# Optimization experiments

Measured on AMD Instinct MI355X. Metric: run time of the kernel, lower is better.

The kernel has to match this reference:

```python
import jax, jax.numpy as jnp
import numpy as np

EPS = 1e-6
NUM_HEADS = 12


def _layernorm(x, eps=EPS):
    m = jnp.mean(x, axis=-1, keepdims=True)
    v = jnp.var(x, axis=-1, keepdims=True)
    return (x - m) * jax.lax.rsqrt(v + eps)


def _rmsnorm(x, w, eps=EPS):
    ms = jnp.mean(jnp.square(x), axis=-1, keepdims=True)
    return x * jax.lax.rsqrt(ms + eps) * w


def _rope_interleaved(x, cos, sin):
    # x: [B, L, H, hd]; cos/sin: [L, hd//2]; is_neox_style=False (interleaved pairs)
    x1 = x[..., 0::2]
    x2 = x[..., 1::2]
    c = cos[None, :, None, :]
    s = sin[None, :, None, :]
    o1 = x1 * c - x2 * s
    o2 = x1 * s + x2 * c
    return jnp.stack([o1, o2], axis=-1).reshape(x.shape)


def _attention(q, k, v, mask=None):
    # q: [B, Lq, H, hd], k/v: [B, Lk, H, hd]
    hd = q.shape[-1]
    scale = 1.0 / jnp.sqrt(jnp.asarray(hd, q.dtype))
    scores = jnp.einsum('blhd,bmhd->bhlm', q, k) * scale
    if mask is not None:
        scores = jnp.where(mask[None, None], scores, jnp.finfo(scores.dtype).min)
    p = jax.nn.softmax(scores, axis=-1)
    return jnp.einsum('bhlm,bmhd->blhd', p, v)


def setup_inputs() -> dict:
    key = jax.random.key(0)
    B, F, FS, D, FF, LC = 1, 2, 1560, 1536, 8960, 512
    L = F * FS
    hd = D // NUM_HEADS
    ks = jax.random.split(key, 32)
    i = iter(range(32))
    n = lambda shape, s=0.02: jax.random.normal(ks[next(i)], shape, jnp.float32) * s
    inp = {
        'hidden_states': n((B, L, D), 1.0),
        'encoder_hidden_states': n((B, LC, D), 1.0),
        'temb': n((B, F, 6, D), 1.0),
    }
    pos = jnp.arange(L, dtype=jnp.float32)
    inv = 1.0 / (10000.0 ** (jnp.arange(hd // 2, dtype=jnp.float32) / (hd // 2)))
    ang = pos[:, None] * inv[None, :]
    inp['cos'] = jnp.cos(ang)
    inp['sin'] = jnp.sin(ang)
    fidx = jnp.arange(L) // FS
    inp['attn_mask'] = fidx[:, None] >= fidx[None, :]  # frame-level block-causal
    # params
    inp['sst'] = n((1, 6, D), 1.0 / np.sqrt(D))
    for name in ['wq', 'wk', 'wv', 'wo']:
        inp[name] = n((D, D))
    for name in ['bq', 'bk', 'bv', 'bo']:
        inp[name] = jnp.zeros((D,), jnp.float32)
    inp['nq_w'] = jnp.ones((D,), jnp.float32)
    inp['nk_w'] = jnp.ones((D,), jnp.float32)
    inp['ln2_g'] = jnp.ones((D,), jnp.float32)
    inp['ln2_b'] = jnp.zeros((D,), jnp.float32)
    for name in ['cwq', 'cwk', 'cwv', 'cwo']:
        inp[name] = n((D, D))
    for name in ['cbq', 'cbk', 'cbv', 'cbo']:
        inp[name] = jnp.zeros((D,), jnp.float32)
    inp['cnq_w'] = jnp.ones((D,), jnp.float32)
    inp['cnk_w'] = jnp.ones((D,), jnp.float32)
    inp['w1'] = n((D, FF))
    inp['b1'] = jnp.zeros((FF,), jnp.float32)
    inp['w2'] = n((FF, D))
    inp['b2'] = jnp.zeros((D,), jnp.float32)
    return inp


def reference(hidden_states, encoder_hidden_states, temb, cos, sin, attn_mask,
              sst, wq, bq, wk, bk, wv, bv, wo, bo, nq_w, nk_w, ln2_g, ln2_b,
              cwq, cbq, cwk, cbk, cwv, cbv, cwo, cbo, cnq_w, cnk_w,
              w1, b1, w2, b2):
    B, L, D = hidden_states.shape
    F = temb.shape[1]
    FS = L // F
    H = NUM_HEADS
    hd = D // H

    e = sst[:, None] + temb  # [B, F, 6, D]
    shift_msa, scale_msa, gate_msa = e[:, :, 0], e[:, :, 1], e[:, :, 2]
    c_shift, c_scale, c_gate = e[:, :, 3], e[:, :, 4], e[:, :, 5]

    # --- self attention ---
    nh = _layernorm(hidden_states).reshape(B, F, FS, D)
    nh = (nh * (1.0 + scale_msa[:, :, None]) + shift_msa[:, :, None]).reshape(B, L, D)
    q = _rmsnorm(nh @ wq + bq, nq_w).reshape(B, L, H, hd)
    k = _rmsnorm(nh @ wk + bk, nk_w).reshape(B, L, H, hd)
    v = (nh @ wv + bv).reshape(B, L, H, hd)
    q = _rope_interleaved(q, cos, sin)
    k = _rope_interleaved(k, cos, sin)
    attn_out = _attention(q, k, v, attn_mask).reshape(B, L, D) @ wo + bo

    h = hidden_states + (attn_out.reshape(B, F, FS, D) * gate_msa[:, :, None]).reshape(B, L, D)
    norm_h = _layernorm(h) * ln2_g + ln2_b  # null shift/scale

    # --- cross attention ---
    LC = encoder_hidden_states.shape[1]
    cq = _rmsnorm(norm_h @ cwq + cbq, cnq_w).reshape(B, L, H, hd)
    ck = _rmsnorm(encoder_hidden_states @ cwk + cbk, cnk_w).reshape(B, LC, H, hd)
    cv = (encoder_hidden_states @ cwv + cbv).reshape(B, LC, H, hd)
    cross_out = _attention(cq, ck, cv).reshape(B, L, D) @ cwo + cbo

    h = h + cross_out  # gate = 1
    norm_h = _layernorm(h).reshape(B, F, FS, D)
    norm_h = (norm_h * (1.0 + c_scale[:, :, None]) + c_shift[:, :, None]).reshape(B, L, D)

    # --- ffn ---
    ff = jax.nn.gelu(norm_h @ w1 + b1, approximate=True) @ w2 + b2
    h = h + (ff.reshape(B, F, FS, D) * c_gate[:, :, None]).reshape(B, L, D)
    return h
```

## Files before the change

### kernel.cpp

```cpp
#include <hip/hip_runtime.h>
#include <hip/hip_bf16.h>
#include <math.h>

typedef __bf16 bf16;
typedef __bf16 bf16x8 __attribute__((ext_vector_type(8)));
typedef float  f32x4  __attribute__((ext_vector_type(4)));
typedef unsigned int u32;

#define DMODEL 1536
#define NHEADS 12
#define HD 128
#define HDH 64

__device__ __forceinline__ void async16(const void* g, void* l) {
  __builtin_amdgcn_global_load_lds((const __attribute__((address_space(1))) u32*)g,
                                   (__attribute__((address_space(3))) u32*)l, 16, 0, 0);
}

__device__ inline void block_reduce2(float& a, float& b) {
  __shared__ float sa[4], sb[4];
  #pragma unroll
  for (int off = 32; off; off >>= 1) {
    a += __shfl_xor(a, off);
    b += __shfl_xor(b, off);
  }
  int w = threadIdx.x >> 6;
  if ((threadIdx.x & 63) == 0) { sa[w] = a; sb[w] = b; }
  __syncthreads();
  a = sa[0] + sa[1] + sa[2] + sa[3];
  b = sb[0] + sb[1] + sb[2] + sb[3];
  __syncthreads();
}

__global__ __launch_bounds__(256)
void ln_kernel(const float* __restrict__ X, bf16* __restrict__ Y,
               const float* __restrict__ sst, const float* __restrict__ temb,
               const float* __restrict__ g, const float* __restrict__ bvec,
               int jshift, int jscale, int FS, int mode)
{
  int row = blockIdx.x;
  const float* x = X + (size_t)row * DMODEL;
  float v[6];
  float s1 = 0.f, s2 = 0.f;
  #pragma unroll
  for (int i = 0; i < 6; i++) {
    float t = x[threadIdx.x + i * 256];
    v[i] = t; s1 += t; s2 += t * t;
  }
  block_reduce2(s1, s2);
  float mean = s1 * (1.f / DMODEL);
  float var  = s2 * (1.f / DMODEL) - mean * mean;
  float rs = rsqrtf(var + 1e-6f);
  int f = row / FS;
  bf16* y = Y + (size_t)row * DMODEL;
  #pragma unroll
  for (int i = 0; i < 6; i++) {
    int d = threadIdx.x + i * 256;
    float t = (v[i] - mean) * rs;
    float o;
    if (mode == 0) {
      float sc = sst[jscale * DMODEL + d] + temb[(f * 6 + jscale) * DMODEL + d];
      float sh = sst[jshift * DMODEL + d] + temb[(f * 6 + jshift) * DMODEL + d];
      o = t * (1.f + sc) + sh;
    } else {
      o = t * g[d] + bvec[d];
    }
    y[d] = (bf16)o;
  }
}

__global__ __launch_bounds__(256)
void rms_rope_kernel(const float* __restrict__ P, int S, long long MN,
                     const bf16* __restrict__ Xb, int RS, int CO,
                     const float* __restrict__ bias, bf16* __restrict__ Y,
                     const float* __restrict__ w,
                     const float* __restrict__ cosb, const float* __restrict__ sinb,
                     int dorope, float oscale)
{
  __shared__ float rowbuf[DMODEL];
  int row = blockIdx.x;
  float v[6];
  float s2 = 0.f, dummy = 0.f;
  if (Xb) {
    const bf16* x = Xb + (size_t)row * RS + CO;
    #pragma unroll
    for (int i = 0; i < 6; i++) {
      int d = threadIdx.x + i * 256;
      float t = (float)x[d];
      v[i] = t; rowbuf[d] = t; s2 += t * t;
    }
  } else {
    const float* x = P + (size_t)row * RS + CO;
    #pragma unroll
    for (int i = 0; i < 6; i++) {
      int d = threadIdx.x + i * 256;
      float t = bias[d];
      for (int s = 0; s < S; s++) t += x[(size_t)s * MN + d];
      v[i] = t; rowbuf[d] = t; s2 += t * t;
    }
  }
  __syncthreads();
  block_reduce2(s2, dummy);
  float rs = rsqrtf(s2 * (1.f / DMODEL) + 1e-6f) * oscale;
  bf16* y = Y + (size_t)row * DMODEL;
  if (dorope) {
    #pragma unroll
    for (int i = 0; i < 3; i++) {
      int p = threadIdx.x + i * 256;
      int d0 = 2 * p, d1 = 2 * p + 1;
      float y0 = rowbuf[d0] * rs * w[d0];
      float y1 = rowbuf[d1] * rs * w[d1];
      int ih = p & 63;
      float c = cosb[(size_t)row * HDH + ih];
      float s = sinb[(size_t)row * HDH + ih];
      y[d0] = (bf16)(y0 * c - y1 * s);
      y[d1] = (bf16)(y0 * s + y1 * c);
    }
  } else {
    #pragma unroll
    for (int i = 0; i < 6; i++) {
      int d = threadIdx.x + i * 256;
      y[d] = (bf16)(v[i] * rs * w[d]);
    }
  }
}

__global__ __launch_bounds__(256)
void wt_kernel(const float* __restrict__ W, bf16* __restrict__ Wt, int K, int N)
{
  __shared__ float T[32][33];
  int k0 = blockIdx.x * 32, n0 = blockIdx.y * 32;
  int tx = threadIdx.x & 31, ty = threadIdx.x >> 5;
  #pragma unroll
  for (int i = 0; i < 4; i++)
    T[ty + 8 * i][tx] = W[(size_t)(k0 + ty + 8 * i) * N + n0 + tx];
  __syncthreads();
  #pragma unroll
  for (int i = 0; i < 4; i++)
    Wt[(size_t)(n0 + ty + 8 * i) * K + k0 + tx] = (bf16)T[tx][ty + 8 * i];
}

__global__ __launch_bounds__(256)
void catbias_kernel(float* __restrict__ bqkv, const float* __restrict__ bq,
                    const float* __restrict__ bk, const float* __restrict__ bv,
                    float* __restrict__ cbkv, const float* __restrict__ cbk,
                    const float* __restrict__ cbv)
{
  int i = blockIdx.x * 256 + threadIdx.x;
  if (i < DMODEL) {
    bqkv[i] = bq[i]; bqkv[DMODEL + i] = bk[i]; bqkv[2 * DMODEL + i] = bv[i];
    cbkv[i] = cbk[i]; cbkv[DMODEL + i] = cbv[i];
  }
}

__global__ __launch_bounds__(256)
void gemm_bt(const bf16* __restrict__ A, const bf16* __restrict__ Bt,
             const float* __restrict__ bias, float* __restrict__ Cf,
             bf16* __restrict__ Cb, int M, int N, int K, int act,
             int Ks, long long MN)
{
  __shared__ bf16 As[128 * 32];
  __shared__ bf16 Bs[128 * 32];
  int tid = threadIdx.x, lane = tid & 63, w = tid >> 6;
  int wm = w >> 1, wn = w & 1;
  int l16 = lane & 15, quad = lane >> 4;

  int gx = (M + 127) >> 7, gy = N >> 7;
  int per_panel = gx << 3;
  int bid = blockIdx.x;
  int panel = bid / per_panel;
  int rem = bid - panel * per_panel;
  int pc0 = panel << 3;
  int ncols = gy - pc0; if (ncols > 8) ncols = 8;
  int by = pc0 + rem % ncols;
  int bx = rem / ncols;
  int bm = bx * 128, bn = by * 128;

  int kb0 = blockIdx.y * Ks;

  int rl = lane >> 2;
  int kk = (lane & 3) * 8;
  int r0 = (2 * w) * 16 + rl, r1 = (2 * w + 1) * 16 + rl;
  int am0 = bm + r0; if (am0 > M - 1) am0 = M - 1;
  int am1 = bm + r1; if (am1 > M - 1) am1 = M - 1;
  const bf16* a0 = A + (size_t)am0 * K + kk;
  const bf16* a1 = A + (size_t)am1 * K + kk;
  const bf16* b0 = Bt + (size_t)(bn + r0) * K + kk;
  const bf16* b1 = Bt + (size_t)(bn + r1) * K + kk;
  bf16* lA0 = As + (2 * w) * 512; bf16* lA1 = As + (2 * w + 1) * 512;
  bf16* lB0 = Bs + (2 * w) * 512; bf16* lB1 = Bs + (2 * w + 1) * 512;

  f32x4 acc[4][4] = {};
  int kend = kb0 + Ks;
  for (int k0 = kb0; k0 < kend; k0 += 32) {
    async16(a0 + k0, lA0);
    async16(a1 + k0, lA1);
    async16(b0 + k0, lB0);
    async16(b1 + k0, lB1);
    __syncthreads();
    bf16x8 af[4], bfv[4];
    #pragma unroll
    for (int mi = 0; mi < 4; mi++)
      af[mi] = *(const bf16x8*)&As[(wm * 64 + mi * 16 + l16) * 32 + quad * 8];
    #pragma unroll
    for (int ni = 0; ni < 4; ni++)
      bfv[ni] = *(const bf16x8*)&Bs[(wn * 64 + ni * 16 + l16) * 32 + quad * 8];
    #pragma unroll
    for (int mi = 0; mi < 4; mi++)
      #pragma unroll
      for (int ni = 0; ni < 4; ni++)
        acc[mi][ni] = __builtin_amdgcn_mfma_f32_16x16x32_bf16(af[mi], bfv[ni], acc[mi][ni], 0, 0, 0);
    __syncthreads();
  }
  float* Cfo = Cf ? Cf + (size_t)blockIdx.y * MN : nullptr;
  #pragma unroll
  for (int mi = 0; mi < 4; mi++) {
    #pragma unroll
    for (int r = 0; r < 4; r++) {
      int m = bm + wm * 64 + mi * 16 + quad * 4 + r;
      if (m < M) {
        #pragma unroll
        for (int ni = 0; ni < 4; ni++) {
          int n = bn + wn * 64 + ni * 16 + l16;
          float val = acc[mi][ni][r] + (bias ? bias[n] : 0.f);
          if (act == 1) {
            float u = val + 0.044715f * val * val * val;
            float z = 1.5957691216057308f * u;
            val = val / (1.f + __expf(-z));
          }
          if (Cfo) Cfo[(size_t)m * N + n] = val;
          else     Cb[(size_t)m * N + n] = (bf16)val;
        }
      }
    }
  }
}

__global__ __launch_bounds__(512, 2)
void gemm256(const bf16* __restrict__ A, const bf16* __restrict__ Bt,
             const float* __restrict__ bias, float* __restrict__ Cf,
             bf16* __restrict__ Cb, int M, int N, int K, int act,
             int S, long long MN)
{
  __shared__ bf16 LDS[2][2][128 * 128];
  int tid = threadIdx.x, lane = tid & 63, w = tid >> 6;
  int wm = w >> 2, wn = w & 3;
  int l16 = lane & 15, quad = lane >> 4;

  int gmx = (M + 255) >> 8, gny = N >> 8;
  int per_panel = gmx << 3;
  int bid = blockIdx.x;
  int panel = bid / per_panel;
  int rem = bid - panel * per_panel;
  int pc0 = panel << 3;
  int ncols = gny - pc0; if (ncols > 8) ncols = 8;
  int by = pc0 + rem % ncols;
  int bx = rem / ncols;
  int bm = bx << 8, bn = by << 8;

  int NTtot = K >> 6;
  int sidx = blockIdx.y;
  int basek = NTtot / S, remk = NTtot % S;
  int NT = basek + (sidx < remk ? 1 : 0);
  int t0k = sidx * basek + (sidx < remk ? sidx : remk);
  int kb0 = t0k << 6;

  int aro = (l16 * 64 + quad * 16) ^ ((l16 >> 3) << 5);
  const char* A0r = (const char*)&LDS[0][0][0] + wm * 16384 + aro;
  const char* A1r = (const char*)&LDS[1][0][0] + wm * 16384 + aro;
  const char* B0r = (const char*)&LDS[0][1][0] + wn * 8192 + aro;
  const char* B1r = (const char*)&LDS[1][1][0] + wn * 8192 + aro;

  int srl = lane >> 2;
  int sc16 = (lane & 3) ^ (((lane >> 5) & 1) << 1);
  int Mm1 = M - 1, Nm1 = N - 1;
  int ga0 = bm + w * 16 + srl;        if (ga0 > Mm1) ga0 = Mm1;
  int ga1 = bm + 128 + w * 16 + srl;  if (ga1 > Mm1) ga1 = Mm1;
  int gb0 = bn + w * 16 + srl;        if (gb0 > Nm1) gb0 = Nm1;
  int gb1 = bn + 128 + w * 16 + srl;  if (gb1 > Nm1) gb1 = Nm1;
  const bf16* Ag0 = A + (size_t)ga0 * K + sc16 * 8;
  const bf16* Ag1 = A + (size_t)ga1 * K + sc16 * 8;
  const bf16* Bg0 = Bt + (size_t)gb0 * K + sc16 * 8;
  const bf16* Bg1 = Bt + (size_t)gb1 * K + sc16 * 8;
  char* wA0[2] = { (char*)&LDS[0][0][0] + w * 2048, (char*)&LDS[1][0][0] + w * 2048 };
  char* wA1[2] = { wA0[0] + 16384, wA0[1] + 16384 };
  char* wB0[2] = { (char*)&LDS[0][1][0] + w * 2048, (char*)&LDS[1][1][0] + w * 2048 };
  char* wB1[2] = { wB0[0] + 16384, wB0[1] + 16384 };

#define STG(src, kk_, dst) do { const bf16* _s = (src) + (kk_); \
    async16(_s, (dst)); async16(_s + 32, (dst) + 1024); } while (0)
#define MFMA_(d, a, b) d = __builtin_amdgcn_mfma_f32_16x16x32_bf16(a, b, d, 0, 0, 0)

  STG(Ag0, kb0, wA0[0]); STG(Ag1, kb0, wA1[0]);
  STG(Bg0, kb0, wB0[0]); STG(Bg1, kb0, wB1[0]);
  if (NT > 1) {
    STG(Bg0, kb0 + 64, wB0[1]); STG(Bg1, kb0 + 64, wB1[1]);
    asm volatile("s_waitcnt vmcnt(4)" ::: "memory");
  } else {
    asm volatile("s_waitcnt vmcnt(0)" ::: "memory");
  }
  __builtin_amdgcn_s_barrier();

  f32x4 acc[8][4] = {};
  for (int t = 0; t < NT; ++t) {
    int b = t & 1;
    const char* Ab = b ? A1r : A0r;
    const char* Bb = b ? B1r : B0r;
    int kt1 = kb0 + (t + 1) * 64;
    int kt2 = kt1 + 64;
    bool st1 = (t + 1) < NT, st2 = (t + 2) < NT;

    bf16x8 a0[8], b0v[4];
    #pragma unroll
    for (int i = 0; i < 8; i++) a0[i] = *(const bf16x8*)(Ab + i * 1024);
    #pragma unroll
    for (int i = 0; i < 4; i++) b0v[i] = *(const bf16x8*)(Bb + i * 1024);
    if (st1) STG(Ag0, kt1, wA0[b ^ 1]);
    __builtin_amdgcn_s_barrier();
    asm volatile("s_waitcnt lgkmcnt(0)" ::: "memory");
    __builtin_amdgcn_s_setprio(1);
    #pragma unroll
    for (int mi = 0; mi < 4; mi++)
      #pragma unroll
      for (int ni = 0; ni < 2; ni++) {
        MFMA_(acc[mi][ni], a0[mi * 2],     b0v[ni * 2]);
        MFMA_(acc[mi][ni], a0[mi * 2 + 1], b0v[ni * 2 + 1]);
      }
    __builtin_amdgcn_s_setprio(0);
    __builtin_amdgcn_s_barrier();

    bf16x8 b1v[4];
    #pragma unroll
    for (int i = 0; i < 4; i++) b1v[i] = *(const bf16x8*)(Bb + (4 + i) * 1024);
    if (st1) STG(Ag1, kt1, wA1[b ^ 1]);
    __builtin_amdgcn_s_barrier();
    asm volatile("s_waitcnt lgkmcnt(0)" ::: "memory");
    __builtin_amdgcn_s_setprio(1);
    #pragma unroll
    for (int mi = 0; mi < 4; mi++)
      #pragma unroll
      for (int ni = 0; ni < 2; ni++) {
        MFMA_(acc[mi][2 + ni], a0[mi * 2],     b1v[ni * 2]);
        MFMA_(acc[mi][2 + ni], a0[mi * 2 + 1], b1v[ni * 2 + 1]);
      }
    __builtin_amdgcn_s_setprio(0);
    __builtin_amdgcn_s_barrier();

    bf16x8 a1[8];
    #pragma unroll
    for (int i = 0; i < 8; i++) a1[i] = *(const bf16x8*)(Ab + (8 + i) * 1024);
    if (st2) STG(Bg0, kt2, wB0[b]);
    __builtin_amdgcn_s_barrier();
    asm volatile("s_waitcnt lgkmcnt(0)" ::: "memory");
    __builtin_amdgcn_s_setprio(1);
    #pragma unroll
    for (int mi = 0; mi < 4; mi++)
      #pragma unroll
      for (int ni = 0; ni < 2; ni++) {
        MFMA_(acc[4 + mi][2 + ni], a1[mi * 2],     b1v[ni * 2]);
        MFMA_(acc[4 + mi][2 + ni], a1[mi * 2 + 1], b1v[ni * 2 + 1]);
      }
    __builtin_amdgcn_s_setprio(0);
    __builtin_amdgcn_s_barrier();

    if (st2) STG(Bg1, kt2, wB1[b]);
    __builtin_amdgcn_s_setprio(1);
    #pragma unroll
    for (int mi = 0; mi < 4; mi++)
      #pragma unroll
      for (int ni = 0; ni < 2; ni++) {
        MFMA_(acc[4 + mi][ni], a1[mi * 2],     b0v[ni * 2]);
        MFMA_(acc[4 + mi][ni], a1[mi * 2 + 1], b0v[ni * 2 + 1]);
      }
    __builtin_amdgcn_s_setprio(0);
    if (st2)      { asm volatile("s_waitcnt vmcnt(4)" ::: "memory"); }
    else if (st1) { asm volatile("s_waitcnt vmcnt(0)" ::: "memory"); }
    __builtin_amdgcn_s_barrier();
  }
#undef STG
#undef MFMA_

  float* Cfo = Cf ? Cf + (size_t)blockIdx.y * MN : nullptr;
  #pragma unroll
  for (int mi = 0; mi < 8; mi++) {
    #pragma unroll
    for (int r = 0; r < 4; r++) {
      int m = bm + wm * 128 + mi * 16 + quad * 4 + r;
      if (m < M) {
        #pragma unroll
        for (int ni = 0; ni < 4; ni++) {
          int n = bn + wn * 64 + ni * 16 + l16;
          float val = acc[mi][ni][r] + (bias ? bias[n] : 0.f);
          if (act == 1) {
            float u = val + 0.044715f * val * val * val;
            float z = 1.5957691216057308f * u;
            val = val / (1.f + __expf(-z));
          }
          if (Cfo) Cfo[(size_t)m * N + n] = val;
          else     Cb[(size_t)m * N + n] = (bf16)val;
        }
      }
    }
  }
}

__global__ __launch_bounds__(256)
void transposev_kernel(const bf16* __restrict__ Xb, int RS, int CO,
                       bf16* __restrict__ Vt, int L)
{
  __shared__ bf16 T[64][65];
  int l0 = blockIdx.x * 64, n0 = blockIdx.y * 64;
  int tid = threadIdx.x;
  int r = tid >> 2;
  int c8 = (tid & 3) * 16;
  int lc = l0 + r; if (lc > L - 1) lc = L - 1;
  const bf16* src = Xb + (size_t)lc * RS + CO + n0 + c8;
  #pragma unroll
  for (int i = 0; i < 16; i++) T[r][c8 + i] = src[i];
  __syncthreads();
  #pragma unroll
  for (int i = 0; i < 16; i++) {
    int l = l0 + c8 + i;
    if (l < L) Vt[(size_t)(n0 + r) * L + l] = T[c8 + i][r];
  }
}

__global__ __launch_bounds__(256)
void flash2_kernel(const bf16* __restrict__ Q, const bf16* __restrict__ Kg,
                   const bf16* __restrict__ Vt, bf16* __restrict__ O,
                   int Lq, int Lk, int FS, int causal, int nqb)
{
  __shared__ bf16 Kt[64 * 128];
  __shared__ bf16 Vtile[128 * 64];
  __shared__ bf16 Pl[4][16][72];
  int tid = threadIdx.x, lane = tid & 63, w = tid >> 6;
  int l16 = lane & 15, quad = lane >> 4;
  int bid = blockIdx.x;
  int h = bid % NHEADS;
  int qb = nqb - 1 - (bid / NHEADS);
  int q0b = qb * 64;
  int q0w = q0b + w * 16;

  int qrow = q0w + l16; if (qrow > Lq - 1) qrow = Lq - 1;
  const bf16* qbase = Q + (size_t)qrow * DMODEL + h * HD + quad * 8;
  bf16x8 qf[4];
  #pragma unroll
  for (int dc = 0; dc < 4; dc++) qf[dc] = *(const bf16x8*)(qbase + dc * 32);

  int kvrow[4];
  int kvmin_w = Lk, kv_end = Lk;
  if (causal) {
    #pragma unroll
    for (int r = 0; r < 4; r++) {
      int qr = q0w + quad * 4 + r; if (qr > Lq - 1) qr = Lq - 1;
      kvrow[r] = (qr / FS + 1) * FS;
    }
    int q0c = q0w; if (q0c > Lq - 1) q0c = Lq - 1;
    kvmin_w = (q0c / FS + 1) * FS;
    int qlast = q0b + 63; if (qlast > Lq - 1) qlast = Lq - 1;
    kv_end = (qlast / FS + 1) * FS;
    if (kv_end > Lk) kv_end = Lk;
  }

  f32x4 acc_o[8] = {};
  float m_i[4], l_i[4];
  #pragma unroll
  for (int r = 0; r < 4; r++) { m_i[r] = -1e30f; l_i[r] = 0.f; }

  for (int kb = 0; kb < kv_end; kb += 64) {
    #pragma unroll
    for (int j = 0; j < 4; j++) {
      int u = w * 256 + j * 64 + lane;
      int row = u >> 4;
      int c = (u & 15) ^ (row & 15);
      int krow = kb + row; if (krow > Lk - 1) krow = Lk - 1;
      async16(Kg + (size_t)krow * DMODEL + h * HD + c * 8,
              Kt + (size_t)(w * 256 + j * 64) * 8);
    }
    #pragma unroll
    for (int j = 0; j < 4; j++) {
      int u = w * 256 + j * 64 + lane;
      int row = u >> 3;
      int c = (u & 7) ^ (row & 7);
      async16(Vt + (size_t)(h * HD + row) * Lk + kb + c * 8,
              Vtile + (size_t)(w * 256 + j * 64) * 8);
    }
    __syncthreads();

    f32x4 s[4] = {};
    #pragma unroll
    for (int nk = 0; nk < 4; nk++) {
      #pragma unroll
      for (int dc = 0; dc < 4; dc++) {
        bf16x8 kf = *(const bf16x8*)&Kt[(((nk * 16 + l16) << 4) + ((4 * dc + quad) ^ l16)) * 8];
        s[nk] = __builtin_amdgcn_mfma_f32_16x16x32_bf16(qf[dc], kf, s[nk], 0, 0, 0);
      }
    }

    bool need_mask = causal && (kb + 64 > kvmin_w);
    float p[4][4];
    #pragma unroll
    for (int r = 0; r < 4; r++) {
      #pragma unroll
      for (int nk = 0; nk < 4; nk++) {
        float sv = s[nk][r];
        if (need_mask && (kb + nk * 16 + l16 >= kvrow[r])) sv = -1e30f;
        p[nk][r] = sv;
      }
      float bm = fmaxf(fmaxf(p[0][r], p[1][r]), fmaxf(p[2][r], p[3][r]));
      #pragma unroll
      for (int off = 8; off; off >>= 1) bm = fmaxf(bm, __shfl_xor(bm, off));
      float mn = fmaxf(m_i[r], bm);
      float alpha = __expf(m_i[r] - mn);
      m_i[r] = mn;
      float ps = 0.f;
      #pragma unroll
      for (int nk = 0; nk < 4; nk++) {
        float e = __expf(p[nk][r] - mn);
        p[nk][r] = e; ps += e;
      }
      #pragma unroll
      for (int off = 8; off; off >>= 1) ps += __shfl_xor(ps, off);
      l_i[r] = l_i[r] * alpha + ps;
      #pragma unroll
      for (int t = 0; t < 8; t++) acc_o[t][r] *= alpha;
    }

    #pragma unroll
    for (int nk = 0; nk < 4; nk++)
      #pragma unroll
      for (int r = 0; r < 4; r++)
        Pl[w][quad * 4 + r][nk * 16 + l16] = (bf16)p[nk][r];
    __threadfence_block();
    bf16x8 pf0 = *(const bf16x8*)&Pl[w][l16][quad * 8];
    bf16x8 pf1 = *(const bf16x8*)&Pl[w][l16][32 + quad * 8];

    #pragma unroll
    for (int t = 0; t < 8; t++) {
      bf16x8 vf0 = *(const bf16x8*)&Vtile[(((t * 16 + l16) << 3) + ((quad) ^ (l16 & 7))) * 8];
      bf16x8 vf1 = *(const bf16x8*)&Vtile[(((t * 16 + l16) << 3) + ((4 + quad) ^ (l16 & 7))) * 8];
      acc_o[t] = __builtin_amdgcn_mfma_f32_16x16x32_bf16(pf0, vf0, acc_o[t], 0, 0, 0);
      acc_o[t] = __builtin_amdgcn_mfma_f32_16x16x32_bf16(pf1, vf1, acc_o[t], 0, 0, 0);
    }
    __syncthreads();
  }

  #pragma unroll
  for (int r = 0; r < 4; r++) {
    int m = q0w + quad * 4 + r;
    if (m < Lq) {
      float inv = 1.f / l_i[r];
      bf16* obase = O + (size_t)m * DMODEL + h * HD;
      #pragma unroll
      for (int t = 0; t < 8; t++)
        obase[t * 16 + l16] = (bf16)(acc_o[t][r] * inv);
    }
  }
}

__global__ __launch_bounds__(256)
void modresid_kernel(const float* __restrict__ base, const float* __restrict__ P,
                     int S, long long MN, const float* __restrict__ bias,
                     float* __restrict__ out,
                     const float* __restrict__ sst, const float* __restrict__ temb,
                     int jg, int FS, long long total)
{
  long long i = (long long)blockIdx.x * 256 + threadIdx.x;
  if (i >= total) return;
  int d = (int)(i % DMODEL);
  int f = (int)((i / DMODEL) / FS);
  float g = sst[jg * DMODEL + d] + temb[(f * 6 + jg) * DMODEL + d];
  float v = bias[d];
  for (int s = 0; s < S; s++) v += P[(size_t)s * MN + i];
  out[i] = base[i] + v * g;
}

__global__ __launch_bounds__(256)
void addf_kernel(float* __restrict__ h, const float* __restrict__ P,
                 int S, long long MN, const float* __restrict__ bias, long long total)
{
  long long i = (long long)blockIdx.x * 256 + threadIdx.x;
  if (i >= total) return;
  int d = (int)(i % DMODEL);
  float v = bias[d];
  for (int s = 0; s < S; s++) v += P[(size_t)s * MN + i];
  h[i] += v;
}

__global__ __launch_bounds__(256)
void cast_kernel(const float* __restrict__ x, bf16* __restrict__ y, long long total)
{
  long long i = (long long)blockIdx.x * 256 + threadIdx.x;
  if (i < total) y[i] = (bf16)x[i];
}

extern "C" void kernel_launch(void* const* d_in, const int* in_sizes, int n_in,
                              void* d_out, int out_size, void* d_ws, size_t ws_size,
                              hipStream_t stream)
{
  const float* hs   = (const float*)d_in[0];
  const float* enc  = (const float*)d_in[1];
  const float* temb = (const float*)d_in[2];
  const float* cosb = (const float*)d_in[3];
  const float* sinb = (const float*)d_in[4];
  const float* sst  = (const float*)d_in[6];
  const float* wq = (const float*)d_in[7];
  const float* wk = (const float*)d_in[8];
  const float* wv = (const float*)d_in[9];
  const float* wo = (const float*)d_in[10];
  const float* bq = (const float*)d_in[11];
  const float* bk = (const float*)d_in[12];
  const float* bv = (const float*)d_in[13];
  const float* bo = (const float*)d_in[14];
  const float* nq_w = (const float*)d_in[15];
  const float* nk_w = (const float*)d_in[16];
  const float* ln2_g = (const float*)d_in[17];
  const float* ln2_b = (const float*)d_in[18];
  const float* cwq = (const float*)d_in[19];
  const float* cwk = (const float*)d_in[20];
  const float* cwv = (const float*)d_in[21];
  const float* cwo = (const float*)d_in[22];
  const float* cbq = (const float*)d_in[23];
  const float* cbk = (const float*)d_in[24];
  const float* cbv = (const float*)d_in[25];
  const float* cbo = (const float*)d_in[26];
  const float* cnq_w = (const float*)d_in[27];
  const float* cnk_w = (const float*)d_in[28];
  const float* w1 = (const float*)d_in[29];
  const float* b1 = (const float*)d_in[30];
  const float* w2 = (const float*)d_in[31];
  const float* b2 = (const float*)d_in[32];

  int L  = in_sizes[0] / DMODEL;
  int LC = in_sizes[1] / DMODEL;
  int F  = in_sizes[2] / (6 * DMODEL);
  int FS = L / F;
  int FF = in_sizes[30];
  long long LD = (long long)L * DMODEL;
  float* outp = (float*)d_out;
  int N3 = 3 * DMODEL, N2 = 2 * DMODEL;

  char* p = (char*)d_ws;
  auto alloc = [&](size_t bytes) -> char* {
    char* r = p; p += (bytes + 255) & ~(size_t)255; return r;
  };
  size_t DD = (size_t)DMODEL * DMODEL;
  bf16* wqkv_t = (bf16*)alloc(DD * 3 * 2);
  bf16* wto_t  = (bf16*)alloc(DD * 2);
  bf16* cwq_t  = (bf16*)alloc(DD * 2);
  bf16* cwkv_t = (bf16*)alloc(DD * 2 * 2);
  bf16* cwo_t  = (bf16*)alloc(DD * 2);
  bf16* w1t = (bf16*)alloc((size_t)DMODEL * FF * 2);
  bf16* w2t = (bf16*)alloc((size_t)DMODEL * FF * 2);
  float* bqkv = (float*)alloc((size_t)N3 * 4);
  float* cbkv = (float*)alloc((size_t)N2 * 4);
  float* hbuf = (float*)alloc((size_t)LD * 4);
  bf16* nh   = (bf16*)alloc((size_t)LD * 2);
  bf16* qb   = (bf16*)alloc((size_t)LD * 2);
  bf16* kb   = (bf16*)alloc((size_t)LD * 2);
  bf16* ab   = (bf16*)alloc((size_t)LD * 2);
  bf16* vtc  = (bf16*)alloc((size_t)LC * DMODEL * 2);
  bf16* encb = (bf16*)alloc((size_t)LC * DMODEL * 2);
  char* BIG1 = alloc((size_t)L * FF * 2);
  bf16* qkvb = (bf16*)BIG1;
  bf16* ckvb = (bf16*)BIG1;
  bf16* ffb  = (bf16*)BIG1;
  char* BIG2 = alloc((size_t)LD * 3 * 4);
  bf16* vtb = (bf16*)BIG2;
  float* Pp = (float*)BIG2;
  (void)ws_size; (void)n_in; (void)out_size;

  dim3 gWdd(DMODEL / 32, DMODEL / 32);
  wt_kernel<<<gWdd, 256, 0, stream>>>(wq, wqkv_t, DMODEL, DMODEL);
  wt_kernel<<<gWdd, 256, 0, stream>>>(wk, wqkv_t + DD, DMODEL, DMODEL);
  wt_kernel<<<gWdd, 256, 0, stream>>>(wv, wqkv_t + 2 * DD, DMODEL, DMODEL);
  wt_kernel<<<gWdd, 256, 0, stream>>>(wo, wto_t, DMODEL, DMODEL);
  wt_kernel<<<gWdd, 256, 0, stream>>>(cwq, cwq_t, DMODEL, DMODEL);
  wt_kernel<<<gWdd, 256, 0, stream>>>(cwk, cwkv_t, DMODEL, DMODEL);
  wt_kernel<<<gWdd, 256, 0, stream>>>(cwv, cwkv_t + DD, DMODEL, DMODEL);
  wt_kernel<<<gWdd, 256, 0, stream>>>(cwo, cwo_t, DMODEL, DMODEL);
  wt_kernel<<<dim3(DMODEL / 32, FF / 32), 256, 0, stream>>>(w1, w1t, DMODEL, FF);
  wt_kernel<<<dim3(FF / 32, DMODEL / 32), 256, 0, stream>>>(w2, w2t, FF, DMODEL);
  catbias_kernel<<<6, 256, 0, stream>>>(bqkv, bq, bk, bv, cbkv, cbk, cbv);

  int gxC = (LC + 127) / 128;
  int gmx = (L + 255) / 256;
  int ewg = (int)((LD + 255) / 256);
  int nqb = (L + 63) / 64;
  const float qs = 0.08838834764831845f;

  ln_kernel<<<L, 256, 0, stream>>>(hs, nh, sst, temb, nullptr, nullptr, 0, 1, FS, 0);
  gemm256<<<dim3(gmx * (N3 / 256), 1), 512, 0, stream>>>(nh, wqkv_t, bqkv, nullptr, qkvb,
                                                         L, N3, DMODEL, 0, 1, 0);
  rms_rope_kernel<<<L, 256, 0, stream>>>(nullptr, 0, 0, qkvb, N3, 0, nullptr, qb, nq_w, cosb, sinb, 1, qs);
  rms_rope_kernel<<<L, 256, 0, stream>>>(nullptr, 0, 0, qkvb, N3, DMODEL, nullptr, kb, nk_w, cosb, sinb, 1, 1.0f);
  transposev_kernel<<<dim3((L + 63) / 64, DMODEL / 64), 256, 0, stream>>>(qkvb, N3, 2 * DMODEL, vtb, L);
  flash2_kernel<<<NHEADS * nqb, 256, 0, stream>>>(qb, kb, vtb, ab, L, L, FS, 1, nqb);
  gemm256<<<dim3(gmx * (DMODEL / 256), 3), 512, 0, stream>>>(ab, wto_t, nullptr, Pp, nullptr,
                                                             L, DMODEL, DMODEL, 0, 3, LD);
  modresid_kernel<<<ewg, 256, 0, stream>>>(hs, Pp, 3, LD, bo, hbuf, sst, temb, 2, FS, LD);
  ln_kernel<<<L, 256, 0, stream>>>(hbuf, nh, nullptr, nullptr, ln2_g, ln2_b, 0, 0, FS, 1);
  gemm256<<<dim3(gmx * (DMODEL / 256), 3), 512, 0, stream>>>(nh, cwq_t, nullptr, Pp, nullptr,
                                                             L, DMODEL, DMODEL, 0, 3, LD);
  rms_rope_kernel<<<L, 256, 0, stream>>>(Pp, 3, LD, nullptr, DMODEL, 0, cbq, qb, cnq_w, nullptr, nullptr, 0, qs);
  cast_kernel<<<(int)(((long long)LC * DMODEL + 255) / 256), 256, 0, stream>>>(enc, encb, (long long)LC * DMODEL);
  gemm_bt<<<dim3(gxC * (N2 / 128), 1), 256, 0, stream>>>(encb, cwkv_t, cbkv, nullptr, ckvb,
                                                         LC, N2, DMODEL, 0, DMODEL, 0);
  rms_rope_kernel<<<LC, 256, 0, stream>>>(nullptr, 0, 0, ckvb, N2, 0, nullptr, kb, cnk_w, nullptr, nullptr, 0, 1.0f);
  transposev_kernel<<<dim3((LC + 63) / 64, DMODEL / 64), 256, 0, stream>>>(ckvb, N2, DMODEL, vtc, LC);
  flash2_kernel<<<NHEADS * nqb, 256, 0, stream>>>(qb, kb, vtc, ab, L, LC, FS, 0, nqb);
  gemm256<<<dim3(gmx * (DMODEL / 256), 3), 512, 0, stream>>>(ab, cwo_t, nullptr, Pp, nullptr,
                                                             L, DMODEL, DMODEL, 0, 3, LD);
  addf_kernel<<<ewg, 256, 0, stream>>>(hbuf, Pp, 3, LD, cbo, LD);
  ln_kernel<<<L, 256, 0, stream>>>(hbuf, nh, sst, temb, nullptr, nullptr, 3, 4, FS, 0);
  gemm256<<<dim3(gmx * (FF / 256), 1), 512, 0, stream>>>(nh, w1t, b1, nullptr, ffb,
                                                         L, FF, DMODEL, 1, 1, 0);
  gemm256<<<dim3(gmx * (DMODEL / 256), 3), 512, 0, stream>>>(ffb, w2t, nullptr, Pp, nullptr,
                                                             L, DMODEL, FF, 0, 3, LD);
  modresid_kernel<<<ewg, 256, 0, stream>>>(hbuf, Pp, 3, LD, b2, outp, sst, temb, 5, FS, LD);
}
```

Measured before the change: 1.113 ms.

## Replace phased GEMM main loop with simple double-buffered prefetch schedule

Result: no change. 1.095 ms (-1.6%).

```diff
diff --git a/kernel.cpp b/kernel.cpp
--- a/kernel.cpp
+++ b/kernel.cpp
@@ -293,12 +293,7 @@
 
   STG(Ag0, kb0, wA0[0]); STG(Ag1, kb0, wA1[0]);
   STG(Bg0, kb0, wB0[0]); STG(Bg1, kb0, wB1[0]);
-  if (NT > 1) {
-    STG(Bg0, kb0 + 64, wB0[1]); STG(Bg1, kb0 + 64, wB1[1]);
-    asm volatile("s_waitcnt vmcnt(4)" ::: "memory");
-  } else {
-    asm volatile("s_waitcnt vmcnt(0)" ::: "memory");
-  }
+  asm volatile("s_waitcnt vmcnt(0)" ::: "memory");
   __builtin_amdgcn_s_barrier();
 
   f32x4 acc[8][4] = {};
@@ -306,75 +301,43 @@
     int b = t & 1;
     const char* Ab = b ? A1r : A0r;
     const char* Bb = b ? B1r : B0r;
-    int kt1 = kb0 + (t + 1) * 64;
-    int kt2 = kt1 + 64;
-    bool st1 = (t + 1) < NT, st2 = (t + 2) < NT;
-
-    bf16x8 a0[8], b0v[4];
+    bool st1 = (t + 1) < NT;
+    if (st1) {
+      int kt = kb0 + (t + 1) * 64;
+      STG(Ag0, kt, wA0[b ^ 1]); STG(Ag1, kt, wA1[b ^ 1]);
+      STG(Bg0, kt, wB0[b ^ 1]); STG(Bg1, kt, wB1[b ^ 1]);
+    }
+    bf16x8 b0v[4], b1v[4], a0[8];
+    #pragma unroll
+    for (int i = 0; i < 4; i++) b0v[i] = *(const bf16x8*)(Bb + i * 1024);
+    #pragma unroll
+    for (int i = 0; i < 4; i++) b1v[i] = *(const bf16x8*)(Bb + (4 + i) * 1024);
     #pragma unroll
     for (int i = 0; i < 8; i++) a0[i] = *(const bf16x8*)(Ab + i * 1024);
     #pragma unroll
-    for (int i = 0; i < 4; i++) b0v[i] = *(const bf16x8*)(Bb + i * 1024);
-    if (st1) STG(Ag0, kt1, wA0[b ^ 1]);
-    __builtin_amdgcn_s_barrier();
-    asm volatile("s_waitcnt lgkmcnt(0)" ::: "memory");
-    __builtin_amdgcn_s_setprio(1);
-    #pragma unroll
-    for (int mi = 0; mi < 4; mi++)
+    for (int mi = 0; mi < 4; mi++) {
       #pragma unroll
       for (int ni = 0; ni < 2; ni++) {
-        MFMA_(acc[mi][ni], a0[mi * 2],     b0v[ni * 2]);
-        MFMA_(acc[mi][ni], a0[mi * 2 + 1], b0v[ni * 2 + 1]);
-      }
-    __builtin_amdgcn_s_setprio(0);
-    __builtin_amdgcn_s_barrier();
-
-    bf16x8 b1v[4];
-    #pragma unroll
-    for (int i = 0; i < 4; i++) b1v[i] = *(const bf16x8*)(Bb + (4 + i) * 1024);
-    if (st1) STG(Ag1, kt1, wA1[b ^ 1]);
-    __builtin_amdgcn_s_barrier();
-    asm volatile("s_waitcnt lgkmcnt(0)" ::: "memory");
-    __builtin_amdgcn_s_setprio(1);
-    #pragma unroll
-    for (int mi = 0; mi < 4; mi++)
-      #pragma unroll
-      for (int ni = 0; ni < 2; ni++) {
+        MFMA_(acc[mi][ni],     a0[mi * 2],     b0v[ni * 2]);
+        MFMA_(acc[mi][ni],     a0[mi * 2 + 1], b0v[ni * 2 + 1]);
         MFMA_(acc[mi][2 + ni], a0[mi * 2],     b1v[ni * 2]);
         MFMA_(acc[mi][2 + ni], a0[mi * 2 + 1], b1v[ni * 2 + 1]);
       }
-    __builtin_amdgcn_s_setprio(0);
-    __builtin_amdgcn_s_barrier();
-
+    }
     bf16x8 a1[8];
     #pragma unroll
     for (int i = 0; i < 8; i++) a1[i] = *(const bf16x8*)(Ab + (8 + i) * 1024);
-    if (st2) STG(Bg0, kt2, wB0[b]);
-    __builtin_amdgcn_s_barrier();
-    asm volatile("s_waitcnt lgkmcnt(0)" ::: "memory");
-    __builtin_amdgcn_s_setprio(1);
-    #pragma unroll
-    for (int mi = 0; mi < 4; mi++)
+    #pragma unroll
+    for (int mi = 0; mi < 4; mi++) {
       #pragma unroll
       for (int ni = 0; ni < 2; ni++) {
+        MFMA_(acc[4 + mi][ni],     a1[mi * 2],     b0v[ni * 2]);
+        MFMA_(acc[4 + mi][ni],     a1[mi * 2 + 1], b0v[ni * 2 + 1]);
         MFMA_(acc[4 + mi][2 + ni], a1[mi * 2],     b1v[ni * 2]);
         MFMA_(acc[4 + mi][2 + ni], a1[mi * 2 + 1], b1v[ni * 2 + 1]);
       }
-    __builtin_amdgcn_s_setprio(0);
-    __builtin_amdgcn_s_barrier();
-
-    if (st2) STG(Bg1, kt2, wB1[b]);
-    __builtin_amdgcn_s_setprio(1);
-    #pragma unroll
-    for (int mi = 0; mi < 4; mi++)
-      #pragma unroll
-      for (int ni = 0; ni < 2; ni++) {
-        MFMA_(acc[4 + mi][ni], a1[mi * 2],     b0v[ni * 2]);
-        MFMA_(acc[4 + mi][ni], a1[mi * 2 + 1], b0v[ni * 2 + 1]);
-      }
-    __builtin_amdgcn_s_setprio(0);
-    if (st2)      { asm volatile("s_waitcnt vmcnt(4)" ::: "memory"); }
-    else if (st1) { asm volatile("s_waitcnt vmcnt(0)" ::: "memory"); }
+    }
+    if (st1) { asm volatile("s_waitcnt vmcnt(0)" ::: "memory"); }
     __builtin_amdgcn_s_barrier();
   }
 #undef STG
```
